# Kernel optimization log

Measured on AMD Instinct MI355X. Metric: run time of the kernel, lower is better.

The kernel has to match this reference:

```python
import jax, jax.numpy as jnp
import numpy as np

NUM_ROUTING_ITERATIONS = 3


def _squash(t, axis=-1):
    # scale * t / ||t||, scale = ||t||^2 / (1 + ||t||^2)
    squared_norm = jnp.sum(t * t, axis=axis, keepdims=True)
    return squared_norm / (1.0 + squared_norm) * t / jnp.sqrt(squared_norm)


def setup_inputs() -> dict:
    key = jax.random.key(0)
    k_x, k_w = jax.random.split(key)
    B, R, C, O, I = 64, 2048, 16, 32, 16
    x = jax.random.normal(k_x, (B, R, I), dtype=jnp.float32)
    W = jax.random.normal(k_w, (R, C, O, I), dtype=jnp.float32)
    return {"x": x, "W": W}


def reference(x, W):
    # u_hat[b,r,c,o] = sum_i W[r,c,o,i] * x[b,r,i]
    u_hat = jnp.einsum('rcoi,bri->brco', W, x)  # [B,R,C,O]
    B, R, C, O = u_hat.shape
    b = jnp.zeros((B, R, C), dtype=u_hat.dtype)  # routing logits
    v = None
    for _ in range(NUM_ROUTING_ITERATIONS):
        c = jax.nn.softmax(b, axis=2)                      # softmax over capsules (dim=2)
        s = jnp.einsum('brc,brco->bro', c, u_hat)          # (c * u_hat).sum(dim=2)
        v = _squash(s, axis=-1)                            # [B,R,O]
        b = b + jnp.einsum('brco,bro->brc', u_hat, v)      # agreement update
    return v
```

## Files before the change

kernel.cpp:

```cpp
#include <hip/hip_runtime.h>

#define R_DIM 2048
#define O_DIM 32
#define I_DIM 16
#define B_DIM 64
#define BB 32

typedef _Float16 half4  __attribute__((ext_vector_type(4)));
typedef float    f32x4  __attribute__((ext_vector_type(4)));

struct SplitH4 { half4 h1, h2; };

__device__ __forceinline__ SplitH4 splitf16x4(const float* __restrict__ p) {
    const float4 f = *(const float4*)p;
    const auto a0 = __builtin_amdgcn_cvt_pkrtz(f.x, f.y);
    const auto a1 = __builtin_amdgcn_cvt_pkrtz(f.z, f.w);
    int ab0, ab1;
    __builtin_memcpy(&ab0, &a0, 4);
    __builtin_memcpy(&ab1, &a1, 4);
    int r0, r1;
    asm("v_fma_mixlo_f16 %0, %1, -1.0, %2 op_sel_hi:[1,0,0]"
        : "=v"(r0) : "v"(ab0), "v"(f.x));
    asm("v_fma_mixhi_f16 %0, %1, -1.0, %2 op_sel:[1,0,0] op_sel_hi:[1,0,0]"
        : "+v"(r0) : "v"(ab0), "v"(f.y));
    asm("v_fma_mixlo_f16 %0, %1, -1.0, %2 op_sel_hi:[1,0,0]"
        : "=v"(r1) : "v"(ab1), "v"(f.z));
    asm("v_fma_mixhi_f16 %0, %1, -1.0, %2 op_sel:[1,0,0] op_sel_hi:[1,0,0]"
        : "+v"(r1) : "v"(ab1), "v"(f.w));
    union U { int i[2]; half4 h; };
    U u1, u2;
    u1.i[0] = ab0; u1.i[1] = ab1;
    u2.i[0] = r0;  u2.i[1] = r1;
    SplitH4 s; s.h1 = u1.h; s.h2 = u2.h;
    return s;
}

template<int CTRL>
__device__ __forceinline__ float dpp_mv(float v) {
    int t = __builtin_amdgcn_update_dpp(0, __float_as_int(v), CTRL, 0xf, 0xf, true);
    return __int_as_float(t);
}
__device__ __forceinline__ float row16_sum(float v) {
    v += dpp_mv<0xB1>(v);
    v += dpp_mv<0x4E>(v);
    v += dpp_mv<0x124>(v);
    v += dpp_mv<0x128>(v);
    return v;
}
__device__ __forceinline__ float row16_max(float v) {
    v = fmaxf(v, dpp_mv<0xB1>(v));
    v = fmaxf(v, dpp_mv<0x4E>(v));
    v = fmaxf(v, dpp_mv<0x124>(v));
    v = fmaxf(v, dpp_mv<0x128>(v));
    return v;
}
__device__ __forceinline__ float ror1(float v) { return dpp_mv<0x121>(v); }
__device__ __forceinline__ float ror2(float v) { return dpp_mv<0x122>(v); }
__device__ __forceinline__ float ror3(float v) { return dpp_mv<0x123>(v); }
__device__ __forceinline__ float ror4(float v) { return dpp_mv<0x124>(v); }

__global__ __launch_bounds__(512, 4)
void capsule_routing_kernel(const float* __restrict__ x,
                            const float* __restrict__ W,
                            float* __restrict__ out) {
    __shared__ float u_lds[BB * 512];

    const int tid = threadIdx.x;
    const int bid = blockIdx.x;
    const int r   = ((bid >> 4) << 3) | (bid & 7);
    const int b0  = ((bid >> 3) & 1) * BB;

    {
        const int lane = tid & 63;
        const int w    = tid >> 6;
        const int q    = lane >> 4;
        const int np   = lane & 15;

        const SplitH4 as0 = splitf16x4(x + ((size_t)(b0 + np)      * R_DIM + r) * I_DIM + q * 4);
        const SplitH4 as1 = splitf16x4(x + ((size_t)(b0 + 16 + np) * R_DIM + r) * I_DIM + q * 4);

        const float* Wbase = W + (size_t)r * 8192 + (size_t)(w * 4) * 256 + np * 16 + q * 4;

        const f32x4 zero4 = {0.f, 0.f, 0.f, 0.f};
        #pragma unroll
        for (int t = 0; t < 4; ++t) {
            const int ntile = w * 4 + t;
            const SplitH4 bs = splitf16x4(Wbase + t * 256);

            const int col = ntile * 16 + np;
            const int v0  = col ^ (q << 3);

            f32x4 a = __builtin_amdgcn_mfma_f32_16x16x16f16(as0.h2, bs.h1, zero4, 0, 0, 0);
            a = __builtin_amdgcn_mfma_f32_16x16x16f16(as0.h1, bs.h2, a, 0, 0, 0);
            a = __builtin_amdgcn_mfma_f32_16x16x16f16(as0.h1, bs.h1, a, 0, 0, 0);
            float* pb = u_lds + q * 2048;
            pb[v0]               = a[0];
            pb[512  + (v0 ^ 8)]  = a[1];
            pb[1024 + (v0 ^ 16)] = a[2];
            pb[1536 + (v0 ^ 24)] = a[3];

            f32x4 c = __builtin_amdgcn_mfma_f32_16x16x16f16(as1.h2, bs.h1, zero4, 0, 0, 0);
            c = __builtin_amdgcn_mfma_f32_16x16x16f16(as1.h1, bs.h2, c, 0, 0, 0);
            c = __builtin_amdgcn_mfma_f32_16x16x16f16(as1.h1, bs.h1, c, 0, 0, 0);
            float* pc = u_lds + 8192 + q * 2048;
            pc[v0]               = c[0];
            pc[512  + (v0 ^ 8)]  = c[1];
            pc[1024 + (v0 ^ 16)] = c[2];
            pc[1536 + (v0 ^ 24)] = c[3];
        }
    }
    __syncthreads();
    __builtin_amdgcn_s_setprio(1);

    {
        const int b = tid >> 4;
        const int j = tid & 15;

        const int sw  = ((b ^ (b >> 2)) & 3) << 3;
        const int pxB = (b * 512 + ((2 * j) ^ sw)) * 4;
        const char* base = (const char*)u_lds;

        float2 X[16];
        {
            int t = j * 128;
            #pragma unroll
            for (int k = 0; k < 16; ++k) {
                X[k] = *(const float2*)(base + ((t & 0x780) | pxB));
                t -= 128;
            }
        }

        float bvv = 0.0f;
        float s0 = 0.f, s1 = 0.f, g = 0.f;

        #pragma unroll
        for (int it = 0; it < 3; ++it) {
            if (it == 0) {
                const float e0 = (X[0].x + X[1].x) + (X[2].x  + X[3].x);
                const float e1 = (X[4].x + X[5].x) + (X[6].x  + X[7].x);
                const float e2 = (X[8].x + X[9].x) + (X[10].x + X[11].x);
                const float e3 = (X[12].x + X[13].x) + (X[14].x + X[15].x);
                const float f0 = (X[0].y + X[1].y) + (X[2].y  + X[3].y);
                const float f1 = (X[4].y + X[5].y) + (X[6].y  + X[7].y);
                const float f2 = (X[8].y + X[9].y) + (X[10].y + X[11].y);
                const float f3 = (X[12].y + X[13].y) + (X[14].y + X[15].y);
                s0 = ((e0 + e1) + (e2 + e3)) * 0.0625f;
                s1 = ((f0 + f1) + (f2 + f3)) * 0.0625f;
            } else {
                const float mx = row16_max(bvv);
                const float e  = exp2f(bvv - mx);
                const float Z  = row16_sum(e);
                const float wr = e * __builtin_amdgcn_rcpf(Z);
                float W0 = wr, W1 = ror1(wr), W2 = ror2(wr), W3 = ror3(wr);
                float sA0 = 0.f, sA1 = 0.f, sB0 = 0.f, sB1 = 0.f;
                float sC0 = 0.f, sC1 = 0.f, sD0 = 0.f, sD1 = 0.f;
                #pragma unroll
                for (int m = 0; m < 4; ++m) {
                    if (m) { W0 = ror4(W0); W1 = ror4(W1); W2 = ror4(W2); W3 = ror4(W3); }
                    sA0 = fmaf(W0, X[4*m].x,     sA0); sA1 = fmaf(W0, X[4*m].y,     sA1);
                    sB0 = fmaf(W1, X[4*m + 1].x, sB0); sB1 = fmaf(W1, X[4*m + 1].y, sB1);
                    sC0 = fmaf(W2, X[4*m + 2].x, sC0); sC1 = fmaf(W2, X[4*m + 2].y, sC1);
                    sD0 = fmaf(W3, X[4*m + 3].x, sD0); sD1 = fmaf(W3, X[4*m + 3].y, sD1);
                }
                s0 = (sA0 + sB0) + (sC0 + sD0);
                s1 = (sA1 + sB1) + (sC1 + sD1);
            }

            const float nn = row16_sum(fmaf(s0, s0, s1 * s1));
            g = sqrtf(nn) * __builtin_amdgcn_rcpf(1.0f + nn);

            if (it < 2) {
                float aA = 0.f, aB = 0.f, aC = 0.f, aD = 0.f;
                #pragma unroll
                for (int m = 0; m < 4; ++m) {
                    if (m) { aA = ror4(aA); aB = ror4(aB); aC = ror4(aC); aD = ror4(aD); }
                    aA = fmaf(X[4*m].x,     s0, aA); aA = fmaf(X[4*m].y,     s1, aA);
                    aB = fmaf(X[4*m + 1].x, s0, aB); aB = fmaf(X[4*m + 1].y, s1, aB);
                    aC = fmaf(X[4*m + 2].x, s0, aC); aC = fmaf(X[4*m + 2].y, s1, aC);
                    aD = fmaf(X[4*m + 3].x, s0, aD); aD = fmaf(X[4*m + 3].y, s1, aD);
                }
                const float acc = (ror4(aA) + ror3(aB)) + (ror2(aC) + ror1(aD));
                bvv = fmaf(g * 1.44269504f, acc, bvv);
            }
        }

        __builtin_amdgcn_s_setprio(0);
        *(float2*)(out + ((size_t)(b0 + b) * R_DIM + r) * O_DIM + 2 * j)
            = make_float2(g * s0, g * s1);
    }
}

extern "C" void kernel_launch(void* const* d_in, const int* in_sizes, int n_in,
                              void* d_out, int out_size, void* d_ws, size_t ws_size,
                              hipStream_t stream) {
    const float* x   = (const float*)d_in[0];
    const float* W   = (const float*)d_in[1];
    float*       out = (float*)d_out;

    dim3 grid(R_DIM * (B_DIM / BB));
    dim3 block(512);
    hipLaunchKernelGGL(capsule_routing_kernel, grid, block, 0, stream, x, W, out);
}
```

Baseline: 122.8 us.

## Process both batch halves per block, overlapping second-half MFMA with first-half routing

Each block now handles one route index r for all 64 batches instead of 32, so the W tile is loaded and split into fp16 halves once and reused for both batch halves. The MFMA products for the second half are interleaved as chunks into the first half's routing iterations after its u values are pulled into registers, so matrix-core work overlaps the scalar routing math. This halves the grid and removes duplicated W traffic, but adds extra barriers and register pressure from holding the four split W fragments, and drops the setprio hints.

```diff
diff --git a/kernel.cpp b/kernel.cpp
--- a/kernel.cpp
+++ b/kernel.cpp
@@ -11,8 +11,7 @@
 
 struct SplitH4 { half4 h1, h2; };
 
-__device__ __forceinline__ SplitH4 splitf16x4(const float* __restrict__ p) {
-    const float4 f = *(const float4*)p;
+__device__ __forceinline__ SplitH4 splitf16v(const float4 f) {
     const auto a0 = __builtin_amdgcn_cvt_pkrtz(f.x, f.y);
     const auto a1 = __builtin_amdgcn_cvt_pkrtz(f.z, f.w);
     int ab0, ab1;
@@ -34,6 +33,9 @@
     SplitH4 s; s.h1 = u1.h; s.h2 = u2.h;
     return s;
 }
+__device__ __forceinline__ SplitH4 splitf16p(const float* __restrict__ p) {
+    return splitf16v(*(const float4*)p);
+}
 
 template<int CTRL>
 __device__ __forceinline__ float dpp_mv(float v) {
@@ -59,135 +61,158 @@
 __device__ __forceinline__ float ror3(float v) { return dpp_mv<0x123>(v); }
 __device__ __forceinline__ float ror4(float v) { return dpp_mv<0x124>(v); }
 
+__device__ __forceinline__ f32x4 mfma3(const SplitH4& A, const SplitH4& B) {
+    const f32x4 z = {0.f, 0.f, 0.f, 0.f};
+    f32x4 a = __builtin_amdgcn_mfma_f32_16x16x16f16(A.h2, B.h1, z, 0, 0, 0);
+    a = __builtin_amdgcn_mfma_f32_16x16x16f16(A.h1, B.h2, a, 0, 0, 0);
+    a = __builtin_amdgcn_mfma_f32_16x16x16f16(A.h1, B.h1, a, 0, 0, 0);
+    return a;
+}
+__device__ __forceinline__ void storeC(float* p, int v0, const f32x4& a) {
+    p[v0]               = a[0];
+    p[512  + (v0 ^ 8)]  = a[1];
+    p[1024 + (v0 ^ 16)] = a[2];
+    p[1536 + (v0 ^ 24)] = a[3];
+}
+
+__device__ __forceinline__ void iter0_mean(const float2* X, float& s0, float& s1) {
+    const float e0 = (X[0].x + X[1].x) + (X[2].x  + X[3].x);
+    const float e1 = (X[4].x + X[5].x) + (X[6].x  + X[7].x);
+    const float e2 = (X[8].x + X[9].x) + (X[10].x + X[11].x);
+    const float e3 = (X[12].x + X[13].x) + (X[14].x + X[15].x);
+    const float f0 = (X[0].y + X[1].y) + (X[2].y  + X[3].y);
+    const float f1 = (X[4].y + X[5].y) + (X[6].y  + X[7].y);
+    const float f2 = (X[8].y + X[9].y) + (X[10].y + X[11].y);
+    const float f3 = (X[12].y + X[13].y) + (X[14].y + X[15].y);
+    s0 = ((e0 + e1) + (e2 + e3)) * 0.0625f;
+    s1 = ((f0 + f1) + (f2 + f3)) * 0.0625f;
+}
+__device__ __forceinline__ float softmax_w(float bvv) {
+    const float mx = row16_max(bvv);
+    const float e  = exp2f(bvv - mx);
+    const float Z  = row16_sum(e);
+    return e * __builtin_amdgcn_rcpf(Z);
+}
+__device__ __forceinline__ void sloop(const float2* X, float wr, float& s0, float& s1) {
+    float W0 = wr, W1 = ror1(wr), W2 = ror2(wr), W3 = ror3(wr);
+    float sA0 = 0.f, sA1 = 0.f, sB0 = 0.f, sB1 = 0.f;
+    float sC0 = 0.f, sC1 = 0.f, sD0 = 0.f, sD1 = 0.f;
+    #pragma unroll
+    for (int m = 0; m < 4; ++m) {
+        if (m) { W0 = ror4(W0); W1 = ror4(W1); W2 = ror4(W2); W3 = ror4(W3); }
+        sA0 = fmaf(W0, X[4*m].x,     sA0); sA1 = fmaf(W0, X[4*m].y,     sA1);
+        sB0 = fmaf(W1, X[4*m + 1].x, sB0); sB1 = fmaf(W1, X[4*m + 1].y, sB1);
+        sC0 = fmaf(W2, X[4*m + 2].x, sC0); sC1 = fmaf(W2, X[4*m + 2].y, sC1);
+        sD0 = fmaf(W3, X[4*m + 3].x, sD0); sD1 = fmaf(W3, X[4*m + 3].y, sD1);
+    }
+    s0 = (sA0 + sB0) + (sC0 + sD0);
+    s1 = (sA1 + sB1) + (sC1 + sD1);
+}
+__device__ __forceinline__ float tloop(const float2* X, float s0, float s1) {
+    float aA = 0.f, aB = 0.f, aC = 0.f, aD = 0.f;
+    #pragma unroll
+    for (int m = 0; m < 4; ++m) {
+        if (m) { aA = ror4(aA); aB = ror4(aB); aC = ror4(aC); aD = ror4(aD); }
+        aA = fmaf(X[4*m].x,     s0, aA); aA = fmaf(X[4*m].y,     s1, aA);
+        aB = fmaf(X[4*m + 1].x, s0, aB); aB = fmaf(X[4*m + 1].y, s1, aB);
+        aC = fmaf(X[4*m + 2].x, s0, aC); aC = fmaf(X[4*m + 2].y, s1, aC);
+        aD = fmaf(X[4*m + 3].x, s0, aD); aD = fmaf(X[4*m + 3].y, s1, aD);
+    }
+    return (ror4(aA) + ror3(aB)) + (ror2(aC) + ror1(aD));
+}
+__device__ __forceinline__ float squash_g(float s0, float s1) {
+    const float nn = row16_sum(fmaf(s0, s0, s1 * s1));
+    return sqrtf(nn) * __builtin_amdgcn_rcpf(1.0f + nn);
+}
+
+template<typename F>
+__device__ __forceinline__ float2 routing_run(const float2* X, F&& chunk) {
+    float s0, s1;
+    chunk(0);
+    iter0_mean(X, s0, s1);
+    float g = squash_g(s0, s1);
+    chunk(1);
+    float bvv = (g * 1.44269504f) * tloop(X, s0, s1);
+    chunk(2);
+    sloop(X, softmax_w(bvv), s0, s1);
+    g = squash_g(s0, s1);
+    chunk(3);
+    bvv = fmaf(g * 1.44269504f, tloop(X, s0, s1), bvv);
+    sloop(X, softmax_w(bvv), s0, s1);
+    g = squash_g(s0, s1);
+    return make_float2(g * s0, g * s1);
+}
+
 __global__ __launch_bounds__(512, 4)
 void capsule_routing_kernel(const float* __restrict__ x,
                             const float* __restrict__ W,
                             float* __restrict__ out) {
     __shared__ float u_lds[BB * 512];
 
-    const int tid = threadIdx.x;
-    const int bid = blockIdx.x;
-    const int r   = ((bid >> 4) << 3) | (bid & 7);
-    const int b0  = ((bid >> 3) & 1) * BB;
-
+    const int tid  = threadIdx.x;
+    const int r    = blockIdx.x;
+    const int lane = tid & 63;
+    const int w4   = (tid >> 6) * 4;
+    const int q    = lane >> 4;
+    const int np   = lane & 15;
+
+    const size_t xrow  = ((size_t)np * R_DIM + r) * I_DIM + q * 4;
+    const size_t bstep = (size_t)16 * R_DIM * I_DIM;
+    const float* Wbase = W + (size_t)r * 8192 + (size_t)w4 * 256 + np * 16 + q * 4;
+
+    const float4 xf1a = *(const float4*)(x + xrow + 2 * bstep);
+    const float4 xf1b = *(const float4*)(x + xrow + 3 * bstep);
+
+    SplitH4 bs[4];
     {
-        const int lane = tid & 63;
-        const int w    = tid >> 6;
-        const int q    = lane >> 4;
-        const int np   = lane & 15;
-
-        const SplitH4 as0 = splitf16x4(x + ((size_t)(b0 + np)      * R_DIM + r) * I_DIM + q * 4);
-        const SplitH4 as1 = splitf16x4(x + ((size_t)(b0 + 16 + np) * R_DIM + r) * I_DIM + q * 4);
-
-        const float* Wbase = W + (size_t)r * 8192 + (size_t)(w * 4) * 256 + np * 16 + q * 4;
-
-        const f32x4 zero4 = {0.f, 0.f, 0.f, 0.f};
+        const SplitH4 as0a = splitf16p(x + xrow);
+        const SplitH4 as0b = splitf16p(x + xrow + bstep);
+        #pragma unroll
+        for (int t = 0; t < 4; ++t) bs[t] = splitf16p(Wbase + t * 256);
         #pragma unroll
         for (int t = 0; t < 4; ++t) {
-            const int ntile = w * 4 + t;
-            const SplitH4 bs = splitf16x4(Wbase + t * 256);
-
-            const int col = ntile * 16 + np;
-            const int v0  = col ^ (q << 3);
-
-            f32x4 a = __builtin_amdgcn_mfma_f32_16x16x16f16(as0.h2, bs.h1, zero4, 0, 0, 0);
-            a = __builtin_amdgcn_mfma_f32_16x16x16f16(as0.h1, bs.h2, a, 0, 0, 0);
-            a = __builtin_amdgcn_mfma_f32_16x16x16f16(as0.h1, bs.h1, a, 0, 0, 0);
-            float* pb = u_lds + q * 2048;
-            pb[v0]               = a[0];
-            pb[512  + (v0 ^ 8)]  = a[1];
-            pb[1024 + (v0 ^ 16)] = a[2];
-            pb[1536 + (v0 ^ 24)] = a[3];
-
-            f32x4 c = __builtin_amdgcn_mfma_f32_16x16x16f16(as1.h2, bs.h1, zero4, 0, 0, 0);
-            c = __builtin_amdgcn_mfma_f32_16x16x16f16(as1.h1, bs.h2, c, 0, 0, 0);
-            c = __builtin_amdgcn_mfma_f32_16x16x16f16(as1.h1, bs.h1, c, 0, 0, 0);
-            float* pc = u_lds + 8192 + q * 2048;
-            pc[v0]               = c[0];
-            pc[512  + (v0 ^ 8)]  = c[1];
-            pc[1024 + (v0 ^ 16)] = c[2];
-            pc[1536 + (v0 ^ 24)] = c[3];
+            const int v0 = ((w4 + t) * 16 + np) ^ (q << 3);
+            storeC(u_lds + q * 2048,        v0, mfma3(as0a, bs[t]));
+            storeC(u_lds + 8192 + q * 2048, v0, mfma3(as0b, bs[t]));
         }
     }
     __syncthreads();
-    __builtin_amdgcn_s_setprio(1);
-
-    {
-        const int b = tid >> 4;
-        const int j = tid & 15;
-
-        const int sw  = ((b ^ (b >> 2)) & 3) << 3;
-        const int pxB = (b * 512 + ((2 * j) ^ sw)) * 4;
-        const char* base = (const char*)u_lds;
-
-        float2 X[16];
-        {
-            int t = j * 128;
-            #pragma unroll
-            for (int k = 0; k < 16; ++k) {
-                X[k] = *(const float2*)(base + ((t & 0x780) | pxB));
-                t -= 128;
-            }
+
+    const int b = tid >> 4;
+    const int j = tid & 15;
+    const int sw  = ((b ^ (b >> 2)) & 3) << 3;
+    const int pxB = (b * 512 + ((2 * j) ^ sw)) * 4;
+    const char* base = (const char*)u_lds;
+
+    #define LOADX(X)                                                   \
+        {                                                              \
+            int tt = j * 128;                                          \
+            _Pragma("unroll")                                          \
+            for (int k = 0; k < 16; ++k) {                             \
+                X[k] = *(const float2*)(base + ((tt & 0x780) | pxB));  \
+                tt -= 128;                                             \
+            }                                                          \
         }
 
-        float bvv = 0.0f;
-        float s0 = 0.f, s1 = 0.f, g = 0.f;
-
-        #pragma unroll
-        for (int it = 0; it < 3; ++it) {
-            if (it == 0) {
-                const float e0 = (X[0].x + X[1].x) + (X[2].x  + X[3].x);
-                const float e1 = (X[4].x + X[5].x) + (X[6].x  + X[7].x);
-                const float e2 = (X[8].x + X[9].x) + (X[10].x + X[11].x);
-                const float e3 = (X[12].x + X[13].x) + (X[14].x + X[15].x);
-                const float f0 = (X[0].y + X[1].y) + (X[2].y  + X[3].y);
-                const float f1 = (X[4].y + X[5].y) + (X[6].y  + X[7].y);
-                const float f2 = (X[8].y + X[9].y) + (X[10].y + X[11].y);
-                const float f3 = (X[12].y + X[13].y) + (X[14].y + X[15].y);
-                s0 = ((e0 + e1) + (e2 + e3)) * 0.0625f;
-                s1 = ((f0 + f1) + (f2 + f3)) * 0.0625f;
-            } else {
-                const float mx = row16_max(bvv);
-                const float e  = exp2f(bvv - mx);
-                const float Z  = row16_sum(e);
-                const float wr = e * __builtin_amdgcn_rcpf(Z);
-                float W0 = wr, W1 = ror1(wr), W2 = ror2(wr), W3 = ror3(wr);
-                float sA0 = 0.f, sA1 = 0.f, sB0 = 0.f, sB1 = 0.f;
-                float sC0 = 0.f, sC1 = 0.f, sD0 = 0.f, sD1 = 0.f;
-                #pragma unroll
-                for (int m = 0; m < 4; ++m) {
-                    if (m) { W0 = ror4(W0); W1 = ror4(W1); W2 = ror4(W2); W3 = ror4(W3); }
-                    sA0 = fmaf(W0, X[4*m].x,     sA0); sA1 = fmaf(W0, X[4*m].y,     sA1);
-                    sB0 = fmaf(W1, X[4*m + 1].x, sB0); sB1 = fmaf(W1, X[4*m + 1].y, sB1);
-                    sC0 = fmaf(W2, X[4*m + 2].x, sC0); sC1 = fmaf(W2, X[4*m + 2].y, sC1);
-                    sD0 = fmaf(W3, X[4*m + 3].x, sD0); sD1 = fmaf(W3, X[4*m + 3].y, sD1);
-                }
-                s0 = (sA0 + sB0) + (sC0 + sD0);
-                s1 = (sA1 + sB1) + (sC1 + sD1);
-            }
-
-            const float nn = row16_sum(fmaf(s0, s0, s1 * s1));
-            g = sqrtf(nn) * __builtin_amdgcn_rcpf(1.0f + nn);
-
-            if (it < 2) {
-                float aA = 0.f, aB = 0.f, aC = 0.f, aD = 0.f;
-                #pragma unroll
-                for (int m = 0; m < 4; ++m) {
-                    if (m) { aA = ror4(aA); aB = ror4(aB); aC = ror4(aC); aD = ror4(aD); }
-                    aA = fmaf(X[4*m].x,     s0, aA); aA = fmaf(X[4*m].y,     s1, aA);
-                    aB = fmaf(X[4*m + 1].x, s0, aB); aB = fmaf(X[4*m + 1].y, s1, aB);
-                    aC = fmaf(X[4*m + 2].x, s0, aC); aC = fmaf(X[4*m + 2].y, s1, aC);
-                    aD = fmaf(X[4*m + 3].x, s0, aD); aD = fmaf(X[4*m + 3].y, s1, aD);
-                }
-                const float acc = (ror4(aA) + ror3(aB)) + (ror2(aC) + ror1(aD));
-                bvv = fmaf(g * 1.44269504f, acc, bvv);
-            }
-        }
-
-        __builtin_amdgcn_s_setprio(0);
-        *(float2*)(out + ((size_t)(b0 + b) * R_DIM + r) * O_DIM + 2 * j)
-            = make_float2(g * s0, g * s1);
-    }
+    float2 X[16];
+    LOADX(X);
+    __syncthreads();
+
+    const SplitH4 as1a = splitf16v(xf1a);
+    const SplitH4 as1b = splitf16v(xf1b);
+    const float2 o0 = routing_run(X, [&](int t) {
+        const int v0 = ((w4 + t) * 16 + np) ^ (q << 3);
+        storeC(u_lds + q * 2048,        v0, mfma3(as1a, bs[t]));
+        storeC(u_lds + 8192 + q * 2048, v0, mfma3(as1b, bs[t]));
+    });
+    *(float2*)(out + ((size_t)b * R_DIM + r) * O_DIM + 2 * j) = o0;
+
+    __syncthreads();
+
+    LOADX(X);
+    const float2 o1 = routing_run(X, [](int) {});
+    *(float2*)(out + ((size_t)(32 + b) * R_DIM + r) * O_DIM + 2 * j) = o1;
+    #undef LOADX
 }
 
 extern "C" void kernel_launch(void* const* d_in, const int* in_sizes, int n_in,
@@ -197,7 +222,7 @@
     const float* W   = (const float*)d_in[1];
     float*       out = (float*)d_out;
 
-    dim3 grid(R_DIM * (B_DIM / BB));
+    dim3 grid(R_DIM);
     dim3 block(512);
     hipLaunchKernelGGL(capsule_routing_kernel, grid, block, 0, stream, x, W, out);
 }
```

New measurement: 120.3 us. 1.02x faster.
